# Kernel optimization log

Hardware: AMD Instinct MI355X
Metric: run time of the kernel (lower is better)

The kernel has to match this reference:

```python
import jax, jax.numpy as jnp
import numpy as np

S, D = 4096, 512      # seq_len, d_model
H, DK = 8, 64         # n_heads, dk == dv
DFF = 2048            # feed-forward hidden
EPS = 1e-5            # torch LayerNorm default eps


def _posenc(seq_len, d_model):
    # Section 3.5 encoding, matching the loop: even i -> sin(pos/10000^(i/d)),
    # odd i -> cos(pos/10000^((i-1)/d)).
    pos = jnp.arange(seq_len, dtype=jnp.float32)[:, None]
    i = jnp.arange(d_model)
    exponent = ((i - (i % 2)).astype(jnp.float32)) / d_model
    ang = pos / jnp.power(jnp.float32(10000.0), exponent)
    return jnp.where(i % 2 == 0, jnp.sin(ang), jnp.cos(ang))


def _layernorm(x, g, b):
    m = jnp.mean(x, axis=-1, keepdims=True)
    v = jnp.mean(jnp.square(x - m), axis=-1, keepdims=True)
    return (x - m) / jnp.sqrt(v + EPS) * g + b


def setup_inputs() -> dict:
    key = jax.random.key(0)
    ks = jax.random.split(key, 9)
    return {
        "E":  jax.random.normal(ks[0], (S, D), jnp.float32),
        # per-head projections stacked over head axis (original: python list of heads)
        "Wq": jax.random.normal(ks[1], (H, D, DK), jnp.float32),
        "Wk": jax.random.normal(ks[2], (H, D, DK), jnp.float32),
        "Wv": jax.random.normal(ks[3], (H, D, DK), jnp.float32),
        "WO": jax.random.normal(ks[4], (H * DK, D), jnp.float32),
        "W1": jax.random.normal(ks[5], (D, DFF), jnp.float32),
        "b1": jax.random.normal(ks[6], (DFF,), jnp.float32),
        "W2": jax.random.normal(ks[7], (DFF, D), jnp.float32),
        "b2": jax.random.normal(ks[8], (D,), jnp.float32),
        # nn.LayerNorm learned affine params (init: weight=1, bias=0)
        "g1": jnp.ones((D,), jnp.float32),
        "be1": jnp.zeros((D,), jnp.float32),
        "g2": jnp.ones((D,), jnp.float32),
        "be2": jnp.zeros((D,), jnp.float32),
    }


def reference(E, Wq, Wk, Wv, WO, W1, b1, W2, b2, g1, be1, g2, be2):
    x = E + _posenc(E.shape[0], E.shape[1])           # (S, D)
    # batched replacement for the per-head python loop
    Q = jnp.einsum('sd,hdk->hsk', x, Wq)              # (H, S, DK)
    K = jnp.einsum('sd,hdk->hsk', x, Wk)
    V = jnp.einsum('sd,hdk->hsk', x, Wv)
    att = jnp.einsum('hsk,htk->hst', Q, K) / jnp.sqrt(jnp.float32(DK))
    Z = jnp.einsum('hst,htv->hsv', jax.nn.softmax(att, axis=-1), V)  # (H,S,DK)
    Zcat = jnp.transpose(Z, (1, 0, 2)).reshape(x.shape[0], H * DK)   # concat heads
    Z1 = _layernorm(Zcat @ WO + x, g1, be1)
    Z2 = jax.nn.relu(Z1 @ W1 + b1) @ W2 + b2
    return _layernorm(Z2 + Z1, g2, be2)
```

## Files before the change

### kernel.cpp

```cpp
#include <hip/hip_runtime.h>
#include <hip/hip_bf16.h>
#include <cmath>

typedef unsigned short u16;
typedef __attribute__((ext_vector_type(8))) short short8;
typedef __attribute__((ext_vector_type(4))) float float4v;
#define LN_EPS 1e-5f

__device__ __forceinline__ float us2f(u16 u) {
    return __uint_as_float(((unsigned int)u) << 16);
}
__device__ __forceinline__ u16 f2us(float f) {
    __hip_bfloat16 h = __float2bfloat16(f);
    return *(u16*)&h;
}

__device__ __forceinline__ float posenc_f(int s, int d) {
    const double c = -9.210340371976184 / 512.0;
    double freq_rev = exp((double)(d & ~1) * c) * 0.15915494309189535;
    double rev = (double)s * freq_rev;
    float fr = (float)(rev - floor(rev));
    float ang = 6.28318530717958647692f * fr;
    return (d & 1) ? __cosf(ang) : __sinf(ang);
}

__global__ __launch_bounds__(256) void sentinel_kernel(float* out, float v) {
    out[blockIdx.x * 256 + threadIdx.x] = v;
}

__global__ __launch_bounds__(256) void qkv10_kernel(const float* __restrict__ E,
                                                    const float* __restrict__ Wq,
                                                    const float* __restrict__ Wk,
                                                    const float* __restrict__ Wv,
                                                    float* __restrict__ Qcat,
                                                    u16* __restrict__ Khi,
                                                    u16* __restrict__ Klo,
                                                    u16* __restrict__ Vt) {
    const int z = blockIdx.y;
    const int type = z >> 3, h = z & 7;
    const float* W = (type == 0 ? Wq : type == 1 ? Wk : Wv) + (long)h * 512 * 64;

    __shared__ u16 sAh[64][72], sAl[64][72];
    __shared__ u16 sBh[64][72], sBl[64][72];
    __shared__ double sFreqRev[512];

    const int t = threadIdx.x;
    const int w = t >> 6, l = t & 63;
    const int quad = l >> 4, l16 = l & 15;
    const int mw = w * 16;
    const int m0 = blockIdx.x * 64;

    {
        const double c = -9.210340371976184 / 512.0;
        sFreqRev[t] = exp((double)(t & ~1) * c) * 0.15915494309189535;
        sFreqRev[t + 256] =
            exp((double)((t + 256) & ~1) * c) * 0.15915494309189535;
    }
    __syncthreads();

    const int ar = t >> 2, ac = (t & 3) << 4;
    const double posd = (double)(m0 + ar);

    float4v acc[4];
    #pragma unroll
    for (int nt = 0; nt < 4; ++nt) acc[nt] = (float4v){0.f, 0.f, 0.f, 0.f};

    for (int k0 = 0; k0 < 512; k0 += 64) {
        #pragma unroll
        for (int u = 0; u < 4; ++u) {
            float4 ev = *(const float4*)(E + (long)(m0 + ar) * 512 + k0 + ac + 4 * u);
            float xs[4] = {ev.x, ev.y, ev.z, ev.w};
            ushort4 hh, ll;
            u16* hp = (u16*)&hh; u16* lp = (u16*)&ll;
            #pragma unroll
            for (int j = 0; j < 4; ++j) {
                const int col = k0 + ac + 4 * u + j;
                double rev = posd * sFreqRev[col];
                float fr = (float)(rev - floor(rev));
                float ang = 6.28318530717958647692f * fr;
                float pe = (j & 1) ? __cosf(ang) : __sinf(ang);
                float x = xs[j] + pe;
                u16 hi = f2us(x);
                hp[j] = hi;
                lp[j] = f2us(x - us2f(hi));
            }
            *(ushort4*)&sAh[ar][ac + 4 * u] = hh;
            *(ushort4*)&sAl[ar][ac + 4 * u] = ll;
        }
        {
            const int kr = t >> 2, nc = (t & 3) << 4;
            #pragma unroll
            for (int u = 0; u < 4; ++u) {
                float4 wv = *(const float4*)(W + (long)(k0 + kr) * 64 + nc + 4 * u);
                float ws4[4] = {wv.x, wv.y, wv.z, wv.w};
                #pragma unroll
                for (int j = 0; j < 4; ++j) {
                    const int n = nc + 4 * u + j;
                    u16 hi = f2us(ws4[j]);
                    sBh[n][kr] = hi;
                    sBl[n][kr] = f2us(ws4[j] - us2f(hi));
                }
            }
        }
        __syncthreads();
        #pragma unroll
        for (int kc = 0; kc < 2; ++kc) {
            short8 ah = *(const short8*)&sAh[mw + l16][kc * 32 + quad * 8];
            short8 al = *(const short8*)&sAl[mw + l16][kc * 32 + quad * 8];
            #pragma unroll
            for (int nt = 0; nt < 4; ++nt) {
                short8 bh = *(const short8*)&sBh[nt * 16 + l16][kc * 32 + quad * 8];
                short8 bl = *(const short8*)&sBl[nt * 16 + l16][kc * 32 + quad * 8];
                acc[nt] = __builtin_amdgcn_mfma_f32_16x16x32_bf16(ah, bh, acc[nt], 0, 0, 0);
                acc[nt] = __builtin_amdgcn_mfma_f32_16x16x32_bf16(ah, bl, acc[nt], 0, 0, 0);
                acc[nt] = __builtin_amdgcn_mfma_f32_16x16x32_bf16(al, bh, acc[nt], 0, 0, 0);
            }
        }
        __syncthreads();
    }

    if (type == 0) {
        #pragma unroll
        for (int nt = 0; nt < 4; ++nt)
            #pragma unroll
            for (int rr = 0; rr < 4; ++rr) {
                const int row = m0 + mw + quad * 4 + rr;
                Qcat[(long)row * 512 + h * 64 + nt * 16 + l16] = acc[nt][rr];
            }
    } else if (type == 1) {
        const int kb = m0 >> 6;
        #pragma unroll
        for (int nt = 0; nt < 4; ++nt) {
            const int fkc = nt >> 1;
            const int fquad = ((nt & 1) << 1) + (l16 >> 3);
            const int fe = l16 & 7;
            const long fbase = ((long)(h * 64 + kb) * 8 + fkc * 4 + w) * 512 +
                               fquad * 128 + fe;
            #pragma unroll
            for (int rr = 0; rr < 4; ++rr) {
                const long off = fbase + (quad * 4 + rr) * 8;
                float v = acc[nt][rr];
                u16 hi = f2us(v);
                Khi[off] = hi;
                Klo[off] = f2us(v - us2f(hi));
            }
        }
    } else {
        const int kb = m0 >> 6;
        const int fkc = w >> 1;
        const int fquad = ((w & 1) << 1) + (quad >> 1);
        const int fe0 = (quad & 1) * 4;
        #pragma unroll
        for (int nt = 0; nt < 4; ++nt) {
            const long off = ((long)(h * 64 + kb) * 8 + fkc * 4 + nt) * 512 +
                             (fquad * 16 + l16) * 8 + fe0;
            ushort4 o;
            o.x = f2us(acc[nt][0]); o.y = f2us(acc[nt][1]);
            o.z = f2us(acc[nt][2]); o.w = f2us(acc[nt][3]);
            *(ushort4*)(Vt + off) = o;
        }
    }
}

__global__ __launch_bounds__(512, 2) void flash14_kernel(const u16* __restrict__ Khi,
                                                         const u16* __restrict__ Klo,
                                                         const u16* __restrict__ Vt,
                                                         float* __restrict__ QZ) {
    const int bid = blockIdx.x;
    const int h = bid & 7;
    const int qb = bid >> 3;

    __shared__ u16 sP[8][64][72];
    __shared__ float mAcc[4][2][4][64][4];
    __shared__ float mML[4][2][2][64];

    const int t = threadIdx.x;
    const int w = t >> 6;
    const int wq = w & 3;
    const int khalf = w >> 2;
    const int l = t & 63;
    const int quad = l >> 4;
    const int l16 = l & 15;
    const int mrow0 = qb * 128 + wq * 32;

    short8 qh[2][2], ql[2][2];
    #pragma unroll
    for (int mf = 0; mf < 2; ++mf)
        #pragma unroll
        for (int kc = 0; kc < 2; ++kc) {
            const float* qp = QZ + (long)(mrow0 + mf * 16 + l16) * 512 + h * 64 +
                              kc * 32 + quad * 8;
            float4 qa = *(const float4*)qp;
            float4 qb4 = *(const float4*)(qp + 4);
            float qv[8] = {qa.x, qa.y, qa.z, qa.w, qb4.x, qb4.y, qb4.z, qb4.w};
            #pragma unroll
            for (int i = 0; i < 8; ++i) {
                float f = qv[i] * 0.125f;
                u16 hi = f2us(f);
                qh[kc][mf][i] = (short)hi;
                ql[kc][mf][i] = (short)f2us(f - us2f(hi));
            }
        }

    const u16* KH = Khi + (long)h * 262144;
    const u16* KL = Klo + (long)h * 262144;
    const u16* VT = Vt + (long)h * 262144;
    const int lo8 = l << 3;
    const int kb0 = khalf * 32;

    float m_i[2] = {-INFINITY, -INFINITY};
    float l_i[2] = {0.0f, 0.0f};
    float4v acc[2][4];
    #pragma unroll
    for (int mf = 0; mf < 2; ++mf)
        #pragma unroll
        for (int nt = 0; nt < 4; ++nt) acc[mf][nt] = (float4v){0.f, 0.f, 0.f, 0.f};

    for (int kb = kb0; kb < kb0 + 32; ++kb) {
        const long fb = (long)kb * 8;
        short8 kh_[8], kl_[8], vv_[8];
        #pragma unroll
        for (int f = 0; f < 8; ++f)
            kh_[f] = *(const short8*)(KH + (fb + f) * 512 + lo8);
        #pragma unroll
        for (int f = 0; f < 8; ++f)
            kl_[f] = *(const short8*)(KL + (fb + f) * 512 + lo8);
        #pragma unroll
        for (int f = 0; f < 8; ++f)
            vv_[f] = *(const short8*)(VT + (fb + f) * 512 + lo8);

        float4v s[2][4];
        #pragma unroll
        for (int mf = 0; mf < 2; ++mf)
            #pragma unroll
            for (int nt = 0; nt < 4; ++nt) s[mf][nt] = (float4v){0.f, 0.f, 0.f, 0.f};

        __builtin_amdgcn_s_setprio(1);
        #pragma unroll
        for (int mf = 0; mf < 2; ++mf) {
            #pragma unroll
            for (int kc = 0; kc < 2; ++kc)
                #pragma unroll
                for (int nt = 0; nt < 4; ++nt)
                    s[mf][nt] = __builtin_amdgcn_mfma_f32_16x16x32_bf16(
                        kh_[kc * 4 + nt], qh[kc][mf], s[mf][nt], 0, 0, 0);
            #pragma unroll
            for (int kc = 0; kc < 2; ++kc)
                #pragma unroll
                for (int nt = 0; nt < 4; ++nt)
                    s[mf][nt] = __builtin_amdgcn_mfma_f32_16x16x32_bf16(
                        kh_[kc * 4 + nt], ql[kc][mf], s[mf][nt], 0, 0, 0);
            #pragma unroll
            for (int kc = 0; kc < 2; ++kc)
                #pragma unroll
                for (int nt = 0; nt < 4; ++nt)
                    s[mf][nt] = __builtin_amdgcn_mfma_f32_16x16x32_bf16(
                        kl_[kc * 4 + nt], qh[kc][mf], s[mf][nt], 0, 0, 0);
        }
        __builtin_amdgcn_s_setprio(0);

        #pragma unroll
        for (int mf = 0; mf < 2; ++mf) {
            float x0 = fmaxf(fmaxf(s[mf][0][0], s[mf][0][1]),
                             fmaxf(s[mf][0][2], s[mf][0][3]));
            float x1 = fmaxf(fmaxf(s[mf][1][0], s[mf][1][1]),
                             fmaxf(s[mf][1][2], s[mf][1][3]));
            float x2 = fmaxf(fmaxf(s[mf][2][0], s[mf][2][1]),
                             fmaxf(s[mf][2][2], s[mf][2][3]));
            float x3 = fmaxf(fmaxf(s[mf][3][0], s[mf][3][1]),
                             fmaxf(s[mf][3][2], s[mf][3][3]));
            float rm = fmaxf(fmaxf(x0, x1), fmaxf(x2, x3));
            rm = fmaxf(rm, __shfl_xor(rm, 16, 64));
            rm = fmaxf(rm, __shfl_xor(rm, 32, 64));
            const float nm = fmaxf(m_i[mf], rm);
            const float al = __expf(m_i[mf] - nm);
            float p[4][4];
            #pragma unroll
            for (int nt = 0; nt < 4; ++nt)
                #pragma unroll
                for (int rr = 0; rr < 4; ++rr)
                    p[nt][rr] = __expf(s[mf][nt][rr] - nm);
            float y0 = (p[0][0] + p[0][1]) + (p[0][2] + p[0][3]);
            float y1 = (p[1][0] + p[1][1]) + (p[1][2] + p[1][3]);
            float y2 = (p[2][0] + p[2][1]) + (p[2][2] + p[2][3]);
            float y3 = (p[3][0] + p[3][1]) + (p[3][2] + p[3][3]);
            float ps = (y0 + y1) + (y2 + y3);
            ps += __shfl_xor(ps, 16, 64);
            ps += __shfl_xor(ps, 32, 64);
            l_i[mf] = l_i[mf] * al + ps;
            m_i[mf] = nm;
            #pragma unroll
            for (int nt = 0; nt < 4; ++nt) {
                acc[mf][nt][0] *= al; acc[mf][nt][1] *= al;
                acc[mf][nt][2] *= al; acc[mf][nt][3] *= al;
            }
            #pragma unroll
            for (int nt = 0; nt < 4; ++nt) {
                ushort4 pk;
                pk.x = f2us(p[nt][0]); pk.y = f2us(p[nt][1]);
                pk.z = f2us(p[nt][2]); pk.w = f2us(p[nt][3]);
                *(ushort4*)&sP[w][mf * 16 + l16][nt * 16 + quad * 4] = pk;
            }
        }

        __builtin_amdgcn_s_setprio(1);
        #pragma unroll
        for (int mf = 0; mf < 2; ++mf)
            #pragma unroll
            for (int kc = 0; kc < 2; ++kc) {
                short8 aP = *(const short8*)&sP[w][mf * 16 + l16][kc * 32 + quad * 8];
                #pragma unroll
                for (int nt = 0; nt < 4; ++nt)
                    acc[mf][nt] = __builtin_amdgcn_mfma_f32_16x16x32_bf16(
                        vv_[kc * 4 + nt], aP, acc[mf][nt], 0, 0, 0);
            }
        __builtin_amdgcn_s_setprio(0);
    }

    if (khalf == 1) {
        #pragma unroll
        for (int mf = 0; mf < 2; ++mf) {
            #pragma unroll
            for (int nt = 0; nt < 4; ++nt)
                *(float4*)&mAcc[wq][mf][nt][l][0] =
                    make_float4(acc[mf][nt][0], acc[mf][nt][1],
                                acc[mf][nt][2], acc[mf][nt][3]);
            mML[wq][mf][0][l] = m_i[mf];
            mML[wq][mf][1][l] = l_i[mf];
        }
    }
    __syncthreads();
    if (khalf == 0) {
        #pragma unroll
        for (int mf = 0; mf < 2; ++mf) {
            const float m1 = mML[wq][mf][0][l];
            const float l1 = mML[wq][mf][1][l];
            const float nm = fmaxf(m_i[mf], m1);
            const float a0 = __expf(m_i[mf] - nm);
            const float a1 = __expf(m1 - nm);
            const float inv = 1.0f / (l_i[mf] * a0 + l1 * a1);
            #pragma unroll
            for (int nt = 0; nt < 4; ++nt) {
                float4 o1 = *(float4*)&mAcc[wq][mf][nt][l][0];
                float4 o = make_float4(
                    (acc[mf][nt][0] * a0 + o1.x * a1) * inv,
                    (acc[mf][nt][1] * a0 + o1.y * a1) * inv,
                    (acc[mf][nt][2] * a0 + o1.z * a1) * inv,
                    (acc[mf][nt][3] * a0 + o1.w * a1) * inv);
                *(float4*)(QZ + (long)(mrow0 + mf * 16 + l16) * 512 + h * 64 +
                           nt * 16 + quad * 4) = o;
            }
        }
    }
}

__global__ __launch_bounds__(256) void wo2_kernel(const float* __restrict__ A,
                                                  const float* __restrict__ B,
                                                  float* __restrict__ C) {
    __shared__ u16 sAh[64][72], sAl[64][72];
    __shared__ u16 sBh[64][72], sBl[64][72];
    const int t = threadIdx.x;
    const int w = t >> 6, l = t & 63;
    const int quad = l >> 4, l16 = l & 15;
    const int mw = w * 16;
    const int m0 = blockIdx.y * 64, n0 = blockIdx.x * 64;
    const int ar = t >> 2, ac = (t & 3) << 4;

    float4v acc[4];
    #pragma unroll
    for (int nt = 0; nt < 4; ++nt) acc[nt] = (float4v){0.f, 0.f, 0.f, 0.f};

    for (int k0 = 0; k0 < 512; k0 += 64) {
        #pragma unroll
        for (int u = 0; u < 4; ++u) {
            float4 av = *(const float4*)(A + (long)(m0 + ar) * 512 + k0 + ac + 4 * u);
            float xs[4] = {av.x, av.y, av.z, av.w};
            ushort4 hh, ll;
            u16* hp = (u16*)&hh; u16* lp = (u16*)&ll;
            #pragma unroll
            for (int j = 0; j < 4; ++j) {
                u16 hi = f2us(xs[j]);
                hp[j] = hi;
                lp[j] = f2us(xs[j] - us2f(hi));
            }
            *(ushort4*)&sAh[ar][ac + 4 * u] = hh;
            *(ushort4*)&sAl[ar][ac + 4 * u] = ll;
        }
        {
            const int kr = t >> 2, nc = (t & 3) << 4;
            #pragma unroll
            for (int u = 0; u < 4; ++u) {
                float4 wv = *(const float4*)(B + (long)(k0 + kr) * 512 + n0 + nc + 4 * u);
                float ws4[4] = {wv.x, wv.y, wv.z, wv.w};
                #pragma unroll
                for (int j = 0; j < 4; ++j) {
                    const int n = nc + 4 * u + j;
                    u16 hi = f2us(ws4[j]);
                    sBh[n][kr] = hi;
                    sBl[n][kr] = f2us(ws4[j] - us2f(hi));
                }
            }
        }
        __syncthreads();
        #pragma unroll
        for (int kc = 0; kc < 2; ++kc) {
            short8 ah = *(const short8*)&sAh[mw + l16][kc * 32 + quad * 8];
            short8 al = *(const short8*)&sAl[mw + l16][kc * 32 + quad * 8];
            #pragma unroll
            for (int nt = 0; nt < 4; ++nt) {
                short8 bh = *(const short8*)&sBh[nt * 16 + l16][kc * 32 + quad * 8];
                short8 bl = *(const short8*)&sBl[nt * 16 + l16][kc * 32 + quad * 8];
                acc[nt] = __builtin_amdgcn_mfma_f32_16x16x32_bf16(ah, bh, acc[nt], 0, 0, 0);
                acc[nt] = __builtin_amdgcn_mfma_f32_16x16x32_bf16(ah, bl, acc[nt], 0, 0, 0);
                acc[nt] = __builtin_amdgcn_mfma_f32_16x16x32_bf16(al, bh, acc[nt], 0, 0, 0);
            }
        }
        __syncthreads();
    }
    #pragma unroll
    for (int nt = 0; nt < 4; ++nt)
        #pragma unroll
        for (int rr = 0; rr < 4; ++rr) {
            const int row = m0 + mw + quad * 4 + rr;
            C[(long)row * 512 + n0 + nt * 16 + l16] = acc[nt][rr];
        }
}

__global__ __launch_bounds__(256) void ln1_kernel(const float* __restrict__ tmp,
                                                  const float* __restrict__ E,
                                                  const float* __restrict__ g,
                                                  const float* __restrict__ be,
                                                  float* __restrict__ out,
                                                  u16* __restrict__ z1b) {
    const int r = blockIdx.x, t = threadIdx.x;
    const long base = (long)r * 512;
    __shared__ float red[256];

    float v0 = tmp[base + t] + E[base + t] + posenc_f(r, t);
    float v1 = tmp[base + t + 256] + E[base + t + 256] + posenc_f(r, t + 256);

    red[t] = v0 + v1; __syncthreads();
    for (int s2 = 128; s2 > 0; s2 >>= 1) {
        if (t < s2) red[t] += red[t + s2];
        __syncthreads();
    }
    const float mean = red[0] * (1.0f / 512.0f);
    __syncthreads();
    float d0 = v0 - mean, d1 = v1 - mean;
    red[t] = d0 * d0 + d1 * d1; __syncthreads();
    for (int s2 = 128; s2 > 0; s2 >>= 1) {
        if (t < s2) red[t] += red[t + s2];
        __syncthreads();
    }
    const float rs = rsqrtf(red[0] * (1.0f / 512.0f) + LN_EPS);
    float o0 = d0 * rs * g[t] + be[t];
    float o1 = d1 * rs * g[t + 256] + be[t + 256];
    out[base + t] = o0;
    out[base + t + 256] = o1;
    z1b[base + t] = f2us(o0);
    z1b[base + t + 256] = f2us(o1);
}

__global__ __launch_bounds__(256) void wtrans_kernel(const float* __restrict__ src,
                                                     u16* __restrict__ dst,
                                                     int K, int N) {
    __shared__ float sT[64][65];
    const int t = threadIdx.x;
    const int k0 = blockIdx.x * 64, n0 = blockIdx.y * 64;
    #pragma unroll
    for (int c = 0; c < 4; ++c) {
        const int r = (t >> 4) + c * 16;
        float4 v = *(const float4*)(src + (long)(k0 + r) * N + n0 + ((t & 15) << 2));
        sT[r][((t & 15) << 2) + 0] = v.x;
        sT[r][((t & 15) << 2) + 1] = v.y;
        sT[r][((t & 15) << 2) + 2] = v.z;
        sT[r][((t & 15) << 2) + 3] = v.w;
    }
    __syncthreads();
    const int n = t >> 2, kc = (t & 3) << 4;
    #pragma unroll
    for (int u = 0; u < 4; ++u) {
        ushort4 o;
        o.x = f2us(sT[kc + 4 * u + 0][n]);
        o.y = f2us(sT[kc + 4 * u + 1][n]);
        o.z = f2us(sT[kc + 4 * u + 2][n]);
        o.w = f2us(sT[kc + 4 * u + 3][n]);
        *(ushort4*)(dst + (long)(n0 + n) * K + k0 + kc + 4 * u) = o;
    }
}

__global__ __launch_bounds__(256) void ffn1_kernel(const u16* __restrict__ A,
                                                   const u16* __restrict__ Bt,
                                                   const float* __restrict__ b1,
                                                   u16* __restrict__ C,
                                                   int m_base) {
    __shared__ u16 sA[64][72], sB[64][72];
    const int t = threadIdx.x;
    const int w = t >> 6, l = t & 63, quad = l >> 4, l16 = l & 15;
    const int mw = w * 16;
    const int m0 = m_base + blockIdx.y * 64, n0 = blockIdx.x * 64;
    const int r = t >> 2, cc = (t & 3) << 4;

    float4v acc[4];
    #pragma unroll
    for (int nt = 0; nt < 4; ++nt) acc[nt] = (float4v){0.f, 0.f, 0.f, 0.f};

    for (int kt = 0; kt < 512; kt += 64) {
        const long aoff = (long)(m0 + r) * 512 + kt + cc;
        *(uint4*)&sA[r][cc]     = *(const uint4*)(A + aoff);
        *(uint4*)&sA[r][cc + 8] = *(const uint4*)(A + aoff + 8);
        const long boff = (long)(n0 + r) * 512 + kt + cc;
        *(uint4*)&sB[r][cc]     = *(const uint4*)(Bt + boff);
        *(uint4*)&sB[r][cc + 8] = *(const uint4*)(Bt + boff + 8);
        __syncthreads();
        #pragma unroll
        for (int kc = 0; kc < 2; ++kc) {
            short8 a = *(const short8*)&sA[mw + l16][kc * 32 + quad * 8];
            #pragma unroll
            for (int nt = 0; nt < 4; ++nt) {
                short8 b = *(const short8*)&sB[nt * 16 + l16][kc * 32 + quad * 8];
                acc[nt] = __builtin_amdgcn_mfma_f32_16x16x32_bf16(a, b, acc[nt], 0, 0, 0);
            }
        }
        __syncthreads();
    }
    #pragma unroll
    for (int rr = 0; rr < 4; ++rr) {
        const int row = blockIdx.y * 64 + mw + quad * 4 + rr;
        #pragma unroll
        for (int nt = 0; nt < 4; ++nt) {
            const int col = n0 + nt * 16 + l16;
            float v = acc[nt][rr] + b1[col];
            C[(long)row * 2048 + col] = f2us(fmaxf(v, 0.0f));
        }
    }
}

__global__ __launch_bounds__(256) void ffn2_kernel(const u16* __restrict__ A,
                                                   const u16* __restrict__ Bt,
                                                   const float* __restrict__ b2,
                                                   float* __restrict__ U) {
    __shared__ u16 sA[64][72], sB[64][72];
    const int t = threadIdx.x;
    const int w = t >> 6, l = t & 63, quad = l >> 4, l16 = l & 15;
    const int mw = w * 16;
    const int m0 = blockIdx.y * 64, n0 = blockIdx.x * 64;
    const int r = t >> 2, cc = (t & 3) << 4;

    float4v acc[4];
    #pragma unroll
    for (int nt = 0; nt < 4; ++nt) acc[nt] = (float4v){0.f, 0.f, 0.f, 0.f};

    for (int kt = 0; kt < 2048; kt += 64) {
        const long aoff = (long)(m0 + r) * 2048 + kt + cc;
        *(uint4*)&sA[r][cc]     = *(const uint4*)(A + aoff);
        *(uint4*)&sA[r][cc + 8] = *(const uint4*)(A + aoff + 8);
        const long boff = (long)(n0 + r) * 2048 + kt + cc;
        *(uint4*)&sB[r][cc]     = *(const uint4*)(Bt + boff);
        *(uint4*)&sB[r][cc + 8] = *(const uint4*)(Bt + boff + 8);
        __syncthreads();
        #pragma unroll
        for (int kc = 0; kc < 2; ++kc) {
            short8 a = *(const short8*)&sA[mw + l16][kc * 32 + quad * 8];
            #pragma unroll
            for (int nt = 0; nt < 4; ++nt) {
                short8 b = *(const short8*)&sB[nt * 16 + l16][kc * 32 + quad * 8];
                acc[nt] = __builtin_amdgcn_mfma_f32_16x16x32_bf16(a, b, acc[nt], 0, 0, 0);
            }
        }
        __syncthreads();
    }
    #pragma unroll
    for (int rr = 0; rr < 4; ++rr) {
        const int row = m0 + mw + quad * 4 + rr;
        #pragma unroll
        for (int nt = 0; nt < 4; ++nt) {
            const int col = n0 + nt * 16 + l16;
            U[(long)row * 512 + col] = acc[nt][rr] + b2[col];
        }
    }
}

__global__ __launch_bounds__(256) void ln2_kernel(const float* __restrict__ U,
                                                  const float* __restrict__ Z1,
                                                  const float* __restrict__ g,
                                                  const float* __restrict__ be,
                                                  float* __restrict__ out) {
    const int r = blockIdx.x, t = threadIdx.x;
    const long base = (long)r * 512;
    __shared__ float red[256];

    float v0 = U[base + t] + Z1[base + t];
    float v1 = U[base + t + 256] + Z1[base + t + 256];

    red[t] = v0 + v1; __syncthreads();
    for (int s2 = 128; s2 > 0; s2 >>= 1) {
        if (t < s2) red[t] += red[t + s2];
        __syncthreads();
    }
    const float mean = red[0] * (1.0f / 512.0f);
    __syncthreads();
    float d0 = v0 - mean, d1 = v1 - mean;
    red[t] = d0 * d0 + d1 * d1; __syncthreads();
    for (int s2 = 128; s2 > 0; s2 >>= 1) {
        if (t < s2) red[t] += red[t + s2];
        __syncthreads();
    }
    const float rs = rsqrtf(red[0] * (1.0f / 512.0f) + LN_EPS);
    out[base + t] = d0 * rs * g[t] + be[t];
    out[base + t + 256] = d1 * rs * g[t + 256] + be[t + 256];
}

extern "C" void kernel_launch(void* const* d_in, const int* in_sizes, int n_in,
                              void* d_out, int out_size, void* d_ws, size_t ws_size,
                              hipStream_t stream) {
    float* outf = (float*)d_out;

    static const int exp_sizes[13] = {2097152, 262144, 262144, 262144, 262144,
                                      1048576, 2048, 1048576, 512, 512, 512,
                                      512, 512};
    bool ok = (n_in == 13) && (out_size == 2097152) &&
              (ws_size >= (14ull << 20));
    if (ok) for (int i = 0; i < 13; ++i) if (in_sizes[i] != exp_sizes[i]) ok = false;
    if (!ok) { sentinel_kernel<<<16, 256, 0, stream>>>(outf, 1000.0f); return; }

    const float* E   = (const float*)d_in[0];
    const float* Wq  = (const float*)d_in[1];
    const float* Wk  = (const float*)d_in[2];
    const float* Wv  = (const float*)d_in[3];
    const float* WO  = (const float*)d_in[4];
    const float* W1  = (const float*)d_in[5];
    const float* b1  = (const float*)d_in[6];
    const float* W2  = (const float*)d_in[7];
    const float* b2  = (const float*)d_in[8];
    const float* g1  = (const float*)d_in[9];
    const float* be1 = (const float*)d_in[10];
    const float* g2  = (const float*)d_in[11];
    const float* be2 = (const float*)d_in[12];

    char* base = (char*)d_ws;
    u16*   Khi = (u16*)base;
    u16*   Klo = (u16*)(base + (4l << 20));
    u16*   Vt  = (u16*)(base + (8l << 20));
    float* tmp = (float*)base;
    u16*   Z1b = (u16*)(base + (8l << 20));
    u16*   W1t = (u16*)base;
    u16*   W2t = (u16*)(base + (2l << 20));
    u16*   Hff = (u16*)(base + (4l << 20));
    float* U   = (float*)(base + (12l << 20));

    qkv10_kernel<<<dim3(64, 24), 256, 0, stream>>>(E, Wq, Wk, Wv, outf,
                                                   Khi, Klo, Vt);
    flash14_kernel<<<dim3(256), 512, 0, stream>>>(Khi, Klo, Vt, outf);
    wo2_kernel<<<dim3(8, 64), 256, 0, stream>>>(outf, WO, tmp);
    ln1_kernel<<<4096, 256, 0, stream>>>(tmp, E, g1, be1, outf, Z1b);
    wtrans_kernel<<<dim3(8, 32), 256, 0, stream>>>(W1, W1t, 512, 2048);
    wtrans_kernel<<<dim3(32, 8), 256, 0, stream>>>(W2, W2t, 2048, 512);

    for (int c = 0; c < 4; ++c) {
        ffn1_kernel<<<dim3(32, 16), 256, 0, stream>>>(Z1b, W1t, b1, Hff,
                                                      c * 1024);
        ffn2_kernel<<<dim3(8, 16), 256, 0, stream>>>(Hff, W2t, b2, U);
        ln2_kernel<<<1024, 256, 0, stream>>>(U, outf + (long)c * 1024 * 512,
                                             g2, be2,
                                             outf + (long)c * 1024 * 512);
    }
}
```

Before: 435.2 us.

## Fuse Q/K/V projections per head and double-buffer K/V tiles in LDS for flash attention

The QKV projection kernel now computes Q, K and V for a head in one block, so the positional-encoding split of E is done once instead of three times, and weight loads are vectorized into LDS. The flash-attention kernel now stages K-hi, K-lo and V tiles cooperatively into a double-buffered LDS buffer. The next tile is prefetched into registers while the current one is computed, replacing per-wave redundant global loads. This raises LDS and register use, cuts the QKV grid to a third, and adds a barrier per iteration.

```diff
diff --git a/kernel.cpp b/kernel.cpp
--- a/kernel.cpp
+++ b/kernel.cpp
@@ -28,7 +28,7 @@
     out[blockIdx.x * 256 + threadIdx.x] = v;
 }
 
-__global__ __launch_bounds__(256) void qkv10_kernel(const float* __restrict__ E,
+__global__ __launch_bounds__(256) void qkv11_kernel(const float* __restrict__ E,
                                                     const float* __restrict__ Wq,
                                                     const float* __restrict__ Wk,
                                                     const float* __restrict__ Wv,
@@ -36,12 +36,13 @@
                                                     u16* __restrict__ Khi,
                                                     u16* __restrict__ Klo,
                                                     u16* __restrict__ Vt) {
-    const int z = blockIdx.y;
-    const int type = z >> 3, h = z & 7;
-    const float* W = (type == 0 ? Wq : type == 1 ? Wk : Wv) + (long)h * 512 * 64;
+    const int h = blockIdx.y;
+    const float* W0 = Wq + (long)h * 512 * 64;
+    const float* W1 = Wk + (long)h * 512 * 64;
+    const float* W2 = Wv + (long)h * 512 * 64;
 
     __shared__ u16 sAh[64][72], sAl[64][72];
-    __shared__ u16 sBh[64][72], sBl[64][72];
+    __shared__ u16 sBh[3][64][72], sBl[3][64][72];
     __shared__ double sFreqRev[512];
 
     const int t = threadIdx.x;
@@ -60,10 +61,14 @@
 
     const int ar = t >> 2, ac = (t & 3) << 4;
     const double posd = (double)(m0 + ar);
-
-    float4v acc[4];
-    #pragma unroll
-    for (int nt = 0; nt < 4; ++nt) acc[nt] = (float4v){0.f, 0.f, 0.f, 0.f};
+    const int brow4 = (t >> 4) << 2;
+    const int bnc = (t & 15) << 2;
+
+    float4v acc[3][4];
+    #pragma unroll
+    for (int ty = 0; ty < 3; ++ty)
+        #pragma unroll
+        for (int nt = 0; nt < 4; ++nt) acc[ty][nt] = (float4v){0.f, 0.f, 0.f, 0.f};
 
     for (int k0 = 0; k0 < 512; k0 += 64) {
         #pragma unroll
@@ -87,19 +92,25 @@
             *(ushort4*)&sAh[ar][ac + 4 * u] = hh;
             *(ushort4*)&sAl[ar][ac + 4 * u] = ll;
         }
-        {
-            const int kr = t >> 2, nc = (t & 3) << 4;
-            #pragma unroll
-            for (int u = 0; u < 4; ++u) {
-                float4 wv = *(const float4*)(W + (long)(k0 + kr) * 64 + nc + 4 * u);
-                float ws4[4] = {wv.x, wv.y, wv.z, wv.w};
+        #pragma unroll
+        for (int ty = 0; ty < 3; ++ty) {
+            const float* W = (ty == 0 ? W0 : ty == 1 ? W1 : W2);
+            float wv4[4][4];
+            #pragma unroll
+            for (int u = 0; u < 4; ++u)
+                *(float4*)&wv4[u][0] =
+                    *(const float4*)(W + (long)(k0 + brow4 + u) * 64 + bnc);
+            #pragma unroll
+            for (int j = 0; j < 4; ++j) {
+                ushort4 hh, ll;
                 #pragma unroll
-                for (int j = 0; j < 4; ++j) {
-                    const int n = nc + 4 * u + j;
-                    u16 hi = f2us(ws4[j]);
-                    sBh[n][kr] = hi;
-                    sBl[n][kr] = f2us(ws4[j] - us2f(hi));
+                for (int u = 0; u < 4; ++u) {
+                    u16 hi = f2us(wv4[u][j]);
+                    ((u16*)&hh)[u] = hi;
+                    ((u16*)&ll)[u] = f2us(wv4[u][j] - us2f(hi));
                 }
+                *(ushort4*)&sBh[ty][bnc + j][brow4] = hh;
+                *(ushort4*)&sBl[ty][bnc + j][brow4] = ll;
             }
         }
         __syncthreads();
@@ -108,26 +119,27 @@
             short8 ah = *(const short8*)&sAh[mw + l16][kc * 32 + quad * 8];
             short8 al = *(const short8*)&sAl[mw + l16][kc * 32 + quad * 8];
             #pragma unroll
-            for (int nt = 0; nt < 4; ++nt) {
-                short8 bh = *(const short8*)&sBh[nt * 16 + l16][kc * 32 + quad * 8];
-                short8 bl = *(const short8*)&sBl[nt * 16 + l16][kc * 32 + quad * 8];
-                acc[nt] = __builtin_amdgcn_mfma_f32_16x16x32_bf16(ah, bh, acc[nt], 0, 0, 0);
-                acc[nt] = __builtin_amdgcn_mfma_f32_16x16x32_bf16(ah, bl, acc[nt], 0, 0, 0);
-                acc[nt] = __builtin_amdgcn_mfma_f32_16x16x32_bf16(al, bh, acc[nt], 0, 0, 0);
-            }
-        }
-        __syncthreads();
-    }
-
-    if (type == 0) {
-        #pragma unroll
-        for (int nt = 0; nt < 4; ++nt)
-            #pragma unroll
-            for (int rr = 0; rr < 4; ++rr) {
-                const int row = m0 + mw + quad * 4 + rr;
-                Qcat[(long)row * 512 + h * 64 + nt * 16 + l16] = acc[nt][rr];
-            }
-    } else if (type == 1) {
+            for (int ty = 0; ty < 3; ++ty)
+                #pragma unroll
+                for (int nt = 0; nt < 4; ++nt) {
+                    short8 bh = *(const short8*)&sBh[ty][nt * 16 + l16][kc * 32 + quad * 8];
+                    short8 bl = *(const short8*)&sBl[ty][nt * 16 + l16][kc * 32 + quad * 8];
+                    acc[ty][nt] = __builtin_amdgcn_mfma_f32_16x16x32_bf16(ah, bh, acc[ty][nt], 0, 0, 0);
+                    acc[ty][nt] = __builtin_amdgcn_mfma_f32_16x16x32_bf16(ah, bl, acc[ty][nt], 0, 0, 0);
+                    acc[ty][nt] = __builtin_amdgcn_mfma_f32_16x16x32_bf16(al, bh, acc[ty][nt], 0, 0, 0);
+                }
+        }
+        __syncthreads();
+    }
+
+    #pragma unroll
+    for (int nt = 0; nt < 4; ++nt)
+        #pragma unroll
+        for (int rr = 0; rr < 4; ++rr) {
+            const int row = m0 + mw + quad * 4 + rr;
+            Qcat[(long)row * 512 + h * 64 + nt * 16 + l16] = acc[0][nt][rr];
+        }
+    {
         const int kb = m0 >> 6;
         #pragma unroll
         for (int nt = 0; nt < 4; ++nt) {
@@ -139,13 +151,14 @@
             #pragma unroll
             for (int rr = 0; rr < 4; ++rr) {
                 const long off = fbase + (quad * 4 + rr) * 8;
-                float v = acc[nt][rr];
+                float v = acc[1][nt][rr];
                 u16 hi = f2us(v);
                 Khi[off] = hi;
                 Klo[off] = f2us(v - us2f(hi));
             }
         }
-    } else {
+    }
+    {
         const int kb = m0 >> 6;
         const int fkc = w >> 1;
         const int fquad = ((w & 1) << 1) + (quad >> 1);
@@ -155,14 +168,14 @@
             const long off = ((long)(h * 64 + kb) * 8 + fkc * 4 + nt) * 512 +
                              (fquad * 16 + l16) * 8 + fe0;
             ushort4 o;
-            o.x = f2us(acc[nt][0]); o.y = f2us(acc[nt][1]);
-            o.z = f2us(acc[nt][2]); o.w = f2us(acc[nt][3]);
+            o.x = f2us(acc[2][nt][0]); o.y = f2us(acc[2][nt][1]);
+            o.z = f2us(acc[2][nt][2]); o.w = f2us(acc[2][nt][3]);
             *(ushort4*)(Vt + off) = o;
         }
     }
 }
 
-__global__ __launch_bounds__(512, 2) void flash14_kernel(const u16* __restrict__ Khi,
+__global__ __launch_bounds__(512, 2) void flash15_kernel(const u16* __restrict__ Khi,
                                                          const u16* __restrict__ Klo,
                                                          const u16* __restrict__ Vt,
                                                          float* __restrict__ QZ) {
@@ -170,9 +183,8 @@
     const int h = bid & 7;
     const int qb = bid >> 3;
 
-    __shared__ u16 sP[8][64][72];
-    __shared__ float mAcc[4][2][4][64][4];
-    __shared__ float mML[4][2][2][64];
+    __shared__ __align__(16) u16 kvbuf[2][2][24][512];
+    __shared__ __align__(16) u16 sP[8][32][72];
 
     const int t = threadIdx.x;
     const int w = t >> 6;
@@ -182,6 +194,7 @@
     const int quad = l >> 4;
     const int l16 = l & 15;
     const int mrow0 = qb * 128 + wq * 32;
+    const int lo8 = l << 3;
 
     short8 qh[2][2], ql[2][2];
     #pragma unroll
@@ -205,7 +218,6 @@
     const u16* KH = Khi + (long)h * 262144;
     const u16* KL = Klo + (long)h * 262144;
     const u16* VT = Vt + (long)h * 262144;
-    const int lo8 = l << 3;
     const int kb0 = khalf * 32;
 
     float m_i[2] = {-INFINITY, -INFINITY};
@@ -216,18 +228,36 @@
         #pragma unroll
         for (int nt = 0; nt < 4; ++nt) acc[mf][nt] = (float4v){0.f, 0.f, 0.f, 0.f};
 
-    for (int kb = kb0; kb < kb0 + 32; ++kb) {
-        const long fb = (long)kb * 8;
-        short8 kh_[8], kl_[8], vv_[8];
-        #pragma unroll
-        for (int f = 0; f < 8; ++f)
-            kh_[f] = *(const short8*)(KH + (fb + f) * 512 + lo8);
-        #pragma unroll
-        for (int f = 0; f < 8; ++f)
-            kl_[f] = *(const short8*)(KL + (fb + f) * 512 + lo8);
-        #pragma unroll
-        for (int f = 0; f < 8; ++f)
-            vv_[f] = *(const short8*)(VT + (fb + f) * 512 + lo8);
+    #pragma unroll
+    for (int j = 0; j < 6; ++j) {
+        const int idx = wq * 6 + j;
+        const int p = idx >> 3, f = idx & 7;
+        const u16* src = (p == 0 ? KH : p == 1 ? KL : VT) +
+                         (long)kb0 * 4096 + f * 512 + lo8;
+        *(uint4*)&kvbuf[khalf][0][idx][lo8] = *(const uint4*)src;
+    }
+    __syncthreads();
+
+    int cur = 0;
+    for (int i = 0; i < 32; ++i) {
+        uint4 stg[6];
+        if (i < 31) {
+            #pragma unroll
+            for (int j = 0; j < 6; ++j) {
+                const int idx = wq * 6 + j;
+                const int p = idx >> 3, f = idx & 7;
+                const u16* src = (p == 0 ? KH : p == 1 ? KL : VT) +
+                                 (long)(kb0 + i + 1) * 4096 + f * 512 + lo8;
+                stg[j] = *(const uint4*)src;
+            }
+        }
+
+        short8 khr[8], klr[8];
+        #pragma unroll
+        for (int f = 0; f < 8; ++f) {
+            khr[f] = *(const short8*)&kvbuf[khalf][cur][f][lo8];
+            klr[f] = *(const short8*)&kvbuf[khalf][cur][8 + f][lo8];
+        }
 
         float4v s[2][4];
         #pragma unroll
@@ -243,19 +273,19 @@
                 #pragma unroll
                 for (int nt = 0; nt < 4; ++nt)
                     s[mf][nt] = __builtin_amdgcn_mfma_f32_16x16x32_bf16(
-                        kh_[kc * 4 + nt], qh[kc][mf], s[mf][nt], 0, 0, 0);
+                        khr[kc * 4 + nt], qh[kc][mf], s[mf][nt], 0, 0, 0);
             #pragma unroll
             for (int kc = 0; kc < 2; ++kc)
                 #pragma unroll
                 for (int nt = 0; nt < 4; ++nt)
                     s[mf][nt] = __builtin_amdgcn_mfma_f32_16x16x32_bf16(
-                        kh_[kc * 4 + nt], ql[kc][mf], s[mf][nt], 0, 0, 0);
+                        khr[kc * 4 + nt], ql[kc][mf], s[mf][nt], 0, 0, 0);
             #pragma unroll
             for (int kc = 0; kc < 2; ++kc)
                 #pragma unroll
                 for (int nt = 0; nt < 4; ++nt)
                     s[mf][nt] = __builtin_amdgcn_mfma_f32_16x16x32_bf16(
-                        kl_[kc * 4 + nt], qh[kc][mf], s[mf][nt], 0, 0, 0);
+                        klr[kc * 4 + nt], qh[kc][mf], s[mf][nt], 0, 0, 0);
         }
         __builtin_amdgcn_s_setprio(0);
 
@@ -303,6 +333,11 @@
             }
         }
 
+        short8 vvr[8];
+        #pragma unroll
+        for (int f = 0; f < 8; ++f)
+            vvr[f] = *(const short8*)&kvbuf[khalf][cur][16 + f][lo8];
+
         __builtin_amdgcn_s_setprio(1);
         #pragma unroll
         for (int mf = 0; mf < 2; ++mf)
@@ -312,36 +347,46 @@
                 #pragma unroll
                 for (int nt = 0; nt < 4; ++nt)
                     acc[mf][nt] = __builtin_amdgcn_mfma_f32_16x16x32_bf16(
-                        vv_[kc * 4 + nt], aP, acc[mf][nt], 0, 0, 0);
+                        vvr[kc * 4 + nt], aP, acc[mf][nt], 0, 0, 0);
             }
         __builtin_amdgcn_s_setprio(0);
-    }
-
+
+        if (i < 31) {
+            #pragma unroll
+            for (int j = 0; j < 6; ++j)
+                *(uint4*)&kvbuf[khalf][cur ^ 1][wq * 6 + j][lo8] = stg[j];
+        }
+        __syncthreads();
+        cur ^= 1;
+    }
+
+    float* mAccF = (float*)&kvbuf[0][0][0][0];
+    float* mMLF = mAccF + 8192;
     if (khalf == 1) {
         #pragma unroll
         for (int mf = 0; mf < 2; ++mf) {
             #pragma unroll
             for (int nt = 0; nt < 4; ++nt)
-                *(float4*)&mAcc[wq][mf][nt][l][0] =
+                *(float4*)&mAccF[(((wq * 2 + mf) * 4 + nt) * 64 + l) * 4] =
                     make_float4(acc[mf][nt][0], acc[mf][nt][1],
                                 acc[mf][nt][2], acc[mf][nt][3]);
-            mML[wq][mf][0][l] = m_i[mf];
-            mML[wq][mf][1][l] = l_i[mf];
+            mMLF[((wq * 2 + mf) * 2 + 0) * 64 + l] = m_i[mf];
+            mMLF[((wq * 2 + mf) * 2 + 1) * 64 + l] = l_i[mf];
         }
     }
     __syncthreads();
     if (khalf == 0) {
         #pragma unroll
         for (int mf = 0; mf < 2; ++mf) {
-            const float m1 = mML[wq][mf][0][l];
-            const float l1 = mML[wq][mf][1][l];
+            const float m1 = mMLF[((wq * 2 + mf) * 2 + 0) * 64 + l];
+            const float l1 = mMLF[((wq * 2 + mf) * 2 + 1) * 64 + l];
             const float nm = fmaxf(m_i[mf], m1);
             const float a0 = __expf(m_i[mf] - nm);
             const float a1 = __expf(m1 - nm);
             const float inv = 1.0f / (l_i[mf] * a0 + l1 * a1);
             #pragma unroll
             for (int nt = 0; nt < 4; ++nt) {
-                float4 o1 = *(float4*)&mAcc[wq][mf][nt][l][0];
+                float4 o1 = *(float4*)&mAccF[(((wq * 2 + mf) * 4 + nt) * 64 + l) * 4];
                 float4 o = make_float4(
                     (acc[mf][nt][0] * a0 + o1.x * a1) * inv,
                     (acc[mf][nt][1] * a0 + o1.y * a1) * inv,
@@ -649,9 +694,9 @@
     u16*   Hff = (u16*)(base + (4l << 20));
     float* U   = (float*)(base + (12l << 20));
 
-    qkv10_kernel<<<dim3(64, 24), 256, 0, stream>>>(E, Wq, Wk, Wv, outf,
-                                                   Khi, Klo, Vt);
-    flash14_kernel<<<dim3(256), 512, 0, stream>>>(Khi, Klo, Vt, outf);
+    qkv11_kernel<<<dim3(64, 8), 256, 0, stream>>>(E, Wq, Wk, Wv, outf,
+                                                  Khi, Klo, Vt);
+    flash15_kernel<<<dim3(256), 512, 0, stream>>>(Khi, Klo, Vt, outf);
     wo2_kernel<<<dim3(8, 64), 256, 0, stream>>>(outf, WO, tmp);
     ln1_kernel<<<4096, 256, 0, stream>>>(tmp, E, g1, be1, outf, Z1b);
     wtrans_kernel<<<dim3(8, 32), 256, 0, stream>>>(W1, W1t, 512, 2048);
```

Result: slower. 481.4 us (+10.6%).
